# Kernel optimization log

Measured on AMD Instinct MI355X. Metric: run time of the kernel, lower is better.

Reference implementation:

```python
import jax, jax.numpy as jnp
import numpy as np

DIM, HEADS = 768, 12
HEAD_DIM = DIM // HEADS
SCALE = HEAD_DIM ** -0.5


def setup_inputs() -> dict:
    key = jax.random.key(0)
    ks = jax.random.split(key, 16)
    B, LQ, LK = 8, 512, 512
    s = DIM ** -0.5
    inp = {
        "query": jax.random.normal(ks[0], (B, LQ, DIM), jnp.float32),
        "key_value": jax.random.normal(ks[1], (B, LK, DIM), jnp.float32),
        "query_coords": jax.random.normal(ks[2], (LQ, 2), jnp.float32),
        "key_coords": jax.random.normal(ks[3], (LK, 2), jnp.float32),
        "Wq": jax.random.normal(ks[4], (DIM, DIM), jnp.float32) * s,
        "bq": jnp.zeros((DIM,), jnp.float32),
        "Wk": jax.random.normal(ks[5], (DIM, DIM), jnp.float32) * s,
        "bk": jnp.zeros((DIM,), jnp.float32),
        "Wv": jax.random.normal(ks[6], (DIM, DIM), jnp.float32) * s,
        "bv": jnp.zeros((DIM,), jnp.float32),
        "Wo": jax.random.normal(ks[7], (DIM, DIM), jnp.float32) * s,
        "bo": jnp.zeros((DIM,), jnp.float32),
        "W1": jax.random.normal(ks[8], (6, DIM), jnp.float32) * (6 ** -0.5),
        "b1": jnp.zeros((DIM,), jnp.float32),
        "W2": jax.random.normal(ks[9], (DIM, HEADS), jnp.float32) * s,
        "b2": jnp.zeros((HEADS,), jnp.float32),
    }
    return inp


def reference(query, key_value, query_coords, key_coords,
              Wq, bq, Wk, bk, Wv, bv, Wo, bo, W1, b1, W2, b2):
    B, LQ, _ = query.shape
    LK = key_value.shape[1]
    # QKV projections -> [B, L, H, Dh]
    q = (query @ Wq + bq).reshape(B, LQ, HEADS, HEAD_DIM)
    k = (key_value @ Wk + bk).reshape(B, LK, HEADS, HEAD_DIM)
    v = (key_value @ Wv + bv).reshape(B, LK, HEADS, HEAD_DIM)
    # attention logits [B, H, LQ, LK]
    logits = jnp.einsum('bqhd,bkhd->bhqk', q, k) * SCALE
    # pairwise relative bias: delta [LQ, LK, 2] -> rel [LQ, LK, 6]
    delta = query_coords[:, None, :] - key_coords[None, :, :]
    rel = jnp.concatenate([delta, jnp.abs(delta), jnp.square(delta)], axis=-1)
    hidden = jax.nn.gelu(rel @ W1 + b1, approximate=False)  # [LQ, LK, DIM]
    bias = hidden @ W2 + b2  # [LQ, LK, H]
    logits = logits + jnp.transpose(bias, (2, 0, 1))[None]  # [B,H,LQ,LK]
    weights = jax.nn.softmax(logits, axis=-1)
    out = jnp.einsum('bhqk,bkhd->bqhd', weights, v).reshape(B, LQ, DIM)
    return out @ Wo + bo
```

## Files before the change

kernel.cpp:

```cpp
#include <hip/hip_runtime.h>
#include <hip/hip_bf16.h>
#include <stdint.h>
#include <math.h>

typedef __attribute__((ext_vector_type(4))) float f32x4;
typedef _Float16 f16;
typedef __attribute__((ext_vector_type(8))) _Float16 f16x8;
typedef decltype(__builtin_amdgcn_cvt_pkrtz(0.f, 0.f)) pk16;

#define DIM   768
#define NH    12
#define HD    64
#define NB    8
#define SEQ   512
#define SCALE 0.125f

#define GN    161
#define GPTS  (GN * GN)

#define MFMA16H __builtin_amdgcn_mfma_f32_16x16x32_f16

struct PrepArgs {
    const float* query; const float* key_value; f16* Xq; f16* Xkv;
    const float* W[4]; f16* WT[4];
    const float* W1; const float* b1; const float* W2;
    f16* W1tab; f16* W2tab; float* gtab32;
};

__global__ void __launch_bounds__(256) k_prep(PrepArgs pa) {
    __shared__ float tt[32][33];
    int g = blockIdx.x, t = threadIdx.x;
    if (g < 3072) {
        const float* in = (g < 1536) ? pa.query : pa.key_value;
        f16* out = (g < 1536) ? pa.Xq : pa.Xkv;
        int i = (g % 1536) * 256 + t;
        const float4* s = reinterpret_cast<const float4*>(in + i * 8);
        float4 f0 = s[0], f1 = s[1];
        union { pk16 h[4]; uint4 v; } o;
        o.h[0] = __builtin_amdgcn_cvt_pkrtz(f0.x, f0.y);
        o.h[1] = __builtin_amdgcn_cvt_pkrtz(f0.z, f0.w);
        o.h[2] = __builtin_amdgcn_cvt_pkrtz(f1.x, f1.y);
        o.h[3] = __builtin_amdgcn_cvt_pkrtz(f1.z, f1.w);
        reinterpret_cast<uint4*>(out)[i] = o.v;
    } else if (g < 5376) {
        int bi = g - 3072;
        int z = bi / 576, rem = bi % 576;
        int bx = rem % 24, by = rem / 24;
        const float* W = pa.W[z];
        f16* WT = pa.WT[z];
        int n0 = bx * 32, k0 = by * 32;
        int tx = t & 31, ty = t >> 5;
#pragma unroll
        for (int j = 0; j < 4; ++j)
            tt[ty + 8 * j][tx] = W[(k0 + ty + 8 * j) * DIM + n0 + tx];
        __syncthreads();
#pragma unroll
        for (int j = 0; j < 4; ++j)
            WT[(n0 + ty + 8 * j) * DIM + k0 + tx] = (f16)tt[tx][ty + 8 * j];
    } else {
        int i = (g - 5376) * 256 + t;
        if (i < 3072) {
            int lane = i & 63;
            int hi = lane >> 4, m = lane & 15;
            int u = (i >> 6) * 16 + m;
#pragma unroll
            for (int e = 0; e < 8; ++e) {
                float v = 0.f;
                if (hi == 0) {
                    if (e < 6) v = pa.W1[e * DIM + u];
                    else if (e == 6) v = pa.b1[u];
                }
                pa.W1tab[i * 8 + e] = (f16)v;
            }
        } else if (i < 4608) {
            int i2 = i - 3072;
            int j = i2 >> 6, lane = i2 & 63;
            int gq = lane >> 4, h = lane & 15;
#pragma unroll
            for (int e = 0; e < 8; ++e) {
                int u = 32 * j + ((e >> 2) << 4) + (gq << 2) + (e & 3);
                float v = (h < 12) ? pa.W2[u * 12 + h] : 0.f;
                pa.W2tab[i2 * 8 + e] = (f16)v;
            }
        } else {
            int i2 = i - 4608;
            float x = (i2 + 0.5f) * (1.0f / 256.0f) - 8.0f;
            pa.gtab32[i2] = 0.5f * x * (1.0f + erff(x * 0.70710678f));
        }
    }
}

__global__ void __launch_bounds__(256) k_grid(const f16x8* __restrict__ W1tab,
                                              const f16x8* __restrict__ W2tab,
                                              const float* __restrict__ b2,
                                              const float* __restrict__ gtab32,
                                              f16* __restrict__ grid16) {
    __shared__ float tab[4096];
    int t = threadIdx.x, lane = t & 63, w = t >> 6;
    {
        const uint4* gt = (const uint4*)gtab32;
        uint4* st = (uint4*)tab;
#pragma unroll
        for (int i = 0; i < 4; ++i) st[i * 256 + t] = gt[i * 256 + t];
    }
    int hi = lane >> 4, m = lane & 15;
    int p0 = blockIdx.x * 64 + w * 16;
    int p = p0 + m;
    int gy = p / GN, gx = p - gy * GN;
    float dx = gx * 0.125f - 10.0f;
    float dy = gy * 0.125f - 10.0f;

    union { f16x8 v; pk16 h2[4]; } rf;
    { f16x8 zz = {}; rf.v = zz; }
    if (hi == 0) {
        rf.h2[0] = __builtin_amdgcn_cvt_pkrtz(dx, dy);
        rf.h2[1] = __builtin_amdgcn_cvt_pkrtz(fabsf(dx), fabsf(dy));
        rf.h2[2] = __builtin_amdgcn_cvt_pkrtz(dx * dx, dy * dy);
        rf.h2[3] = __builtin_amdgcn_cvt_pkrtz(1.0f, 0.0f);
    }

    float b2h = (m < 12) ? b2[m] : 0.f;
    f32x4 acc = {b2h, b2h, b2h, b2h};
    const f32x4 zero = {};
    const f16x8* w1p = W1tab + lane;
    const f16x8* w2p = W2tab + lane;
    __syncthreads();

#pragma unroll 2
    for (int j = 0; j < 24; ++j) {
        f16x8 a0  = w1p[(2 * j) * 64];
        f16x8 a1  = w1p[(2 * j + 1) * 64];
        f16x8 w2v = w2p[j * 64];
        f32x4 pre0 = MFMA16H(a0, rf.v, zero, 0, 0, 0);
        f32x4 pre1 = MFMA16H(a1, rf.v, zero, 0, 0, 0);
        float s0[4], s1[4];
#pragma unroll
        for (int e = 0; e < 4; ++e) {
            float x0 = pre0[e];
            float xi0 = __builtin_amdgcn_fmed3f(__builtin_fmaf(x0, 256.f, 2048.f), 0.f, 4095.f);
            float g0 = tab[(int)xi0];
            s0[e] = (x0 > 8.f) ? x0 : g0;
            float x1 = pre1[e];
            float xi1 = __builtin_amdgcn_fmed3f(__builtin_fmaf(x1, 256.f, 2048.f), 0.f, 4095.f);
            float g1 = tab[(int)xi1];
            s1[e] = (x1 > 8.f) ? x1 : g1;
        }
        union { f16x8 v; pk16 h2[4]; } pav;
        pav.h2[0] = __builtin_amdgcn_cvt_pkrtz(s0[0], s0[1]);
        pav.h2[1] = __builtin_amdgcn_cvt_pkrtz(s0[2], s0[3]);
        pav.h2[2] = __builtin_amdgcn_cvt_pkrtz(s1[0], s1[1]);
        pav.h2[3] = __builtin_amdgcn_cvt_pkrtz(s1[2], s1[3]);
        acc = MFMA16H(pav.v, w2v, acc, 0, 0, 0);
    }
    if (m < 12) {
#pragma unroll
        for (int r = 0; r < 4; ++r) {
            int pr = p0 + hi * 4 + r;
            if (pr < GPTS) grid16[pr * 16 + m] = (f16)acc[r];
        }
    }
}

struct MQArgs {
    const float* qc; const float* kc;
    const f16* grid16; f16* bias16;
    const f16* Xq; const f16* Xkv;
    const f16* WqT; const f16* WkT; const f16* WvT;
    const float* bq; const float* bk; const float* bv;
    f16* q_ws; f16* k_ws; f16* v_t;
};

__global__ void __launch_bounds__(256) k_mq5(MQArgs a) {
    __shared__ uint4 lds[1024];
    int bid = blockIdx.x, t = threadIdx.x;
    int lane = t & 63, w = t >> 6;
    int hi = lane >> 4, lm = lane & 15;
    int xcd = bid & 7, slot = bid >> 3;

    if (slot >= 16) {
        int lid = xcd * 288 + (slot - 16);
        int m_group = lid / 36;
        int within = lid - m_group * 36;
        int z = within / 12;
        int n_tile = within - z * 12;
        int m0 = m_group * 64, n0 = n_tile * 64;
        const f16* X = (z == 0) ? a.Xq : a.Xkv;
        const f16* Wt = (z == 0) ? a.WqT : (z == 1) ? a.WkT : a.WvT;
        const float* bias = (z == 0) ? a.bq : (z == 1) ? a.bk : a.bv;
        f16* out = (z == 0) ? a.q_ws : (z == 1) ? a.k_ws : a.v_t;

        int wr = w >> 1, wc = w & 1;
        int srow = t >> 2, sslot = t & 3;
        const f16* Ag = X + (m0 + srow) * DIM + sslot * 8;
        const f16* Bg = Wt + (n0 + srow) * DIM + sslot * 8;
        int wi = srow * 4 + (sslot ^ ((srow >> 1) & 3));

        int aidx[2], bidx[2];
#pragma unroll
        for (int i = 0; i < 2; ++i) {
            int ar = wr * 32 + i * 16 + lm;
            aidx[i] = ar * 4 + (hi ^ ((ar >> 1) & 3));
            int br = wc * 32 + i * 16 + lm;
            bidx[i] = 256 + br * 4 + (hi ^ ((br >> 1) & 3));
        }

        f32x4 acc[2][2] = {};
        {
            uint4 a0 = *(const uint4*)(Ag);
            uint4 b0 = *(const uint4*)(Bg);
            lds[wi] = a0;
            lds[256 + wi] = b0;
        }
        uint4 sA1 = *(const uint4*)(Ag + 32);
        uint4 sB1 = *(const uint4*)(Bg + 32);
        uint4 sA0 = *(const uint4*)(Ag + 64);
        uint4 sB0 = *(const uint4*)(Bg + 64);
        __syncthreads();

#define MQ_COMPUTE(kt)                                                        \
        {                                                                     \
            int bo = ((kt) & 1) << 9;                                         \
            f16x8 af0 = *(const f16x8*)&lds[bo + aidx[0]];                    \
            f16x8 af1 = *(const f16x8*)&lds[bo + aidx[1]];                    \
            f16x8 bf0 = *(const f16x8*)&lds[bo + bidx[0]];                    \
            f16x8 bf1 = *(const f16x8*)&lds[bo + bidx[1]];                    \
            acc[0][0] = MFMA16H(af0, bf0, acc[0][0], 0, 0, 0);                \
            acc[0][1] = MFMA16H(af0, bf1, acc[0][1], 0, 0, 0);                \
            acc[1][0] = MFMA16H(af1, bf0, acc[1][0], 0, 0, 0);                \
            acc[1][1] = MFMA16H(af1, bf1, acc[1][1], 0, 0, 0);                \
        }

        for (int kp = 0; kp < 12; ++kp) {
            int kt = 2 * kp;
            MQ_COMPUTE(kt)
            {
                int bo2 = (((kt) & 1) << 9) ^ 512;
                lds[bo2 + wi] = sA1;
                lds[bo2 + 256 + wi] = sB1;
                if (kt + 3 < 24) {
                    sA1 = *(const uint4*)(Ag + (kt + 3) * 32);
                    sB1 = *(const uint4*)(Bg + (kt + 3) * 32);
                }
                __syncthreads();
            }
            kt = 2 * kp + 1;
            MQ_COMPUTE(kt)
            if (kt < 23) {
                int bo2 = (((kt) & 1) << 9) ^ 512;
                lds[bo2 + wi] = sA0;
                lds[bo2 + 256 + wi] = sB0;
                if (kt + 3 < 24) {
                    sA0 = *(const uint4*)(Ag + (kt + 3) * 32);
                    sB0 = *(const uint4*)(Bg + (kt + 3) * 32);
                }
                __syncthreads();
            }
        }
#undef MQ_COMPUTE

#pragma unroll
        for (int mi = 0; mi < 2; ++mi)
#pragma unroll
            for (int ni = 0; ni < 2; ++ni) {
                int n = n0 + wc * 32 + ni * 16 + lm;
                float bn = bias[n];
                int h = n >> 6, d = n & 63;
                int mbase = m0 + wr * 32 + mi * 16 + hi * 4;
                int bb = mbase >> 9, l0 = mbase & 511;
                if (z == 2) {
                    union { pk16 h2[2]; uint2 u2; } o;
                    o.h2[0] = __builtin_amdgcn_cvt_pkrtz(acc[mi][ni][0] + bn, acc[mi][ni][1] + bn);
                    o.h2[1] = __builtin_amdgcn_cvt_pkrtz(acc[mi][ni][2] + bn, acc[mi][ni][3] + bn);
                    *reinterpret_cast<uint2*>(out + (((bb * NH + h) * HD) + d) * SEQ + l0) = o.u2;
                } else {
#pragma unroll
                    for (int r = 0; r < 4; ++r)
                        out[(((bb * NH + h) * SEQ) + l0 + r) * HD + d] = (f16)(acc[mi][ni][r] + bn);
                }
            }
    } else {
        int id = xcd * 16 + slot;
#pragma unroll 2
        for (int i = 0; i < 8; ++i) {
            int p = id * 2048 + i * 256 + t;
            int qi = p >> 9, ki = p & 511;
            float dx = a.qc[2 * qi] - a.kc[2 * ki];
            float dy = a.qc[2 * qi + 1] - a.kc[2 * ki + 1];
            float fxf = __builtin_amdgcn_fmed3f(__builtin_fmaf(dx, 8.f, 80.f), 0.f, 159.9999f);
            float fyf = __builtin_amdgcn_fmed3f(__builtin_fmaf(dy, 8.f, 80.f), 0.f, 159.9999f);
            int ix = (int)fxf, iy = (int)fyf;
            float fx = fxf - (float)ix, fy = fyf - (float)iy;
            const f16* c00 = a.grid16 + (iy * GN + ix) * 16;
            f16x8 g00 = *(const f16x8*)(c00);
            f16x8 g00b = *(const f16x8*)(c00 + 8);
            f16x8 g01 = *(const f16x8*)(c00 + 16);
            f16x8 g01b = *(const f16x8*)(c00 + 24);
            f16x8 g10 = *(const f16x8*)(c00 + GN * 16);
            f16x8 g10b = *(const f16x8*)(c00 + GN * 16 + 8);
            f16x8 g11 = *(const f16x8*)(c00 + GN * 16 + 16);
            f16x8 g11b = *(const f16x8*)(c00 + GN * 16 + 24);
            float o[12];
#pragma unroll
            for (int h = 0; h < 12; ++h) {
                float v00 = (float)(h < 8 ? g00[h] : g00b[h - 8]);
                float v01 = (float)(h < 8 ? g01[h] : g01b[h - 8]);
                float v10 = (float)(h < 8 ? g10[h] : g10b[h - 8]);
                float v11 = (float)(h < 8 ? g11[h] : g11b[h - 8]);
                float v0 = __builtin_fmaf(fx, v01 - v00, v00);
                float v1 = __builtin_fmaf(fx, v11 - v10, v10);
                o[h] = __builtin_fmaf(fy, v1 - v0, v0);
            }
#pragma unroll
            for (int h = 0; h < 12; ++h)
                a.bias16[h * (SEQ * SEQ) + p] = (f16)o[h];
        }
    }
}

__global__ void __launch_bounds__(256) k_gemmO(const f16* __restrict__ X,
                                               const f16* __restrict__ WT,
                                               const float* __restrict__ bias,
                                               float* __restrict__ out) {
    __shared__ uint4 lds[2048];
    int bid = blockIdx.x;
    int xcd = bid & 7, slot = bid >> 3;
    int m0 = (xcd * 4 + slot / 6) * 128, n0 = (slot % 6) * 128;
    int t = threadIdx.x, lane = t & 63, w = t >> 6;
    int wr = w >> 1, wc = w & 1;
    int lm = lane & 15, hi = lane >> 4;

    int srow = t >> 1, sch = t & 1;
    const f16* Ag = X + (m0 + srow) * DIM + sch * 16;
    const f16* Bg = WT + (n0 + srow) * DIM + sch * 16;
    int sw = (srow >> 1) & 3;
    int wiA0 = srow * 4 + ((2 * sch) ^ sw);
    int wiA1 = srow * 4 + ((2 * sch + 1) ^ sw);

    int aidx[4], bidx[4];
#pragma unroll
    for (int i = 0; i < 4; ++i) {
        int ar = wr * 64 + i * 16 + lm;
        aidx[i] = ar * 4 + (hi ^ ((ar >> 1) & 3));
        int br = wc * 64 + i * 16 + lm;
        bidx[i] = 512 + br * 4 + (hi ^ ((br >> 1) & 3));
    }

    f32x4 acc[4][4] = {};
    {
        lds[wiA0] = *(const uint4*)(Ag);
        lds[wiA1] = *(const uint4*)(Ag + 8);
        lds[512 + wiA0] = *(const uint4*)(Bg);
        lds[512 + wiA1] = *(const uint4*)(Bg + 8);
    }
    __syncthreads();

    for (int kt = 0; kt < 24; ++kt) {
        uint4 na0, na1, nb0, nb1;
        bool pf = kt < 23;
        if (pf) {
            const f16* An = Ag + (kt + 1) * 32;
            const f16* Bn = Bg + (kt + 1) * 32;
            na0 = *(const uint4*)(An);
            na1 = *(const uint4*)(An + 8);
            nb0 = *(const uint4*)(Bn);
            nb1 = *(const uint4*)(Bn + 8);
        }
        int bo = (kt & 1) << 10;
        f16x8 af[4], bf[4];
#pragma unroll
        for (int i = 0; i < 4; ++i) {
            af[i] = *(const f16x8*)&lds[bo + aidx[i]];
            bf[i] = *(const f16x8*)&lds[bo + bidx[i]];
        }
#pragma unroll
        for (int mi = 0; mi < 4; ++mi)
#pragma unroll
            for (int ni = 0; ni < 4; ++ni)
                acc[mi][ni] = MFMA16H(af[mi], bf[ni], acc[mi][ni], 0, 0, 0);
        if (pf) {
            int bo2 = bo ^ 1024;
            lds[bo2 + wiA0] = na0; lds[bo2 + wiA1] = na1;
            lds[bo2 + 512 + wiA0] = nb0; lds[bo2 + 512 + wiA1] = nb1;
            __syncthreads();
        }
    }

#pragma unroll
    for (int mi = 0; mi < 4; ++mi)
#pragma unroll
        for (int ni = 0; ni < 4; ++ni) {
            int n = n0 + wc * 64 + ni * 16 + lm;
            float bn = bias[n];
#pragma unroll
            for (int r = 0; r < 4; ++r) {
                int m = m0 + wr * 64 + mi * 16 + hi * 4 + r;
                out[m * DIM + n] = acc[mi][ni][r] + bn;
            }
        }
}

__global__ void __launch_bounds__(256) k_attn4(const f16* __restrict__ q_ws,
                                               const f16* __restrict__ k_ws,
                                               const f16* __restrict__ v_t,
                                               const f16* __restrict__ bias16,
                                               f16* __restrict__ attn_out) {
    __shared__ __align__(16) unsigned short sm16[32 * 520];
    __shared__ float inv32[32];
    int bid = blockIdx.x;
    int xcd = bid & 7, slot = bid >> 3;
    int g = xcd * 12 + (slot >> 4);
    int h = g % 12, b = g / 12;
    int qt = slot & 15;
    int q0 = qt * 32;
    int t = threadIdx.x, lane = t & 63, w = t >> 6;
    int lrow = lane & 15, hi = lane >> 4;
    int bh = b * NH + h;
    const f16* Q = q_ws + (bh * SEQ + q0) * HD;
    const f16* K = k_ws + bh * SEQ * HD;
    const f16* Bias = bias16 + (h * SEQ + q0) * SEQ;

    f16x8 aq[2][2];
#pragma unroll
    for (int rt = 0; rt < 2; ++rt)
#pragma unroll
        for (int ds = 0; ds < 2; ++ds) {
            f16x8 v = *(const f16x8*)(Q + (rt * 16 + lrow) * HD + ds * 32 + hi * 8);
            aq[rt][ds] = v * (f16)SCALE;
        }

#pragma unroll
    for (int ct = 0; ct < 8; ++ct) {
        f32x4 acc0 = {}, acc1 = {};
        int kk = w * 128 + ct * 16 + lrow;
#pragma unroll
        for (int ds = 0; ds < 2; ++ds) {
            f16x8 bk = *(const f16x8*)(K + kk * HD + ds * 32 + hi * 8);
            acc0 = MFMA16H(aq[0][ds], bk, acc0, 0, 0, 0);
            acc1 = MFMA16H(aq[1][ds], bk, acc1, 0, 0, 0);
        }
#pragma unroll
        for (int r = 0; r < 4; ++r) {
            int row0 = hi * 4 + r;
            sm16[row0 * 520 + kk] = (unsigned short)__builtin_bit_cast(unsigned short,
                (f16)(acc0[r] + (float)Bias[row0 * SEQ + kk]));
            int row1 = 16 + hi * 4 + r;
            sm16[row1 * 520 + kk] = (unsigned short)__builtin_bit_cast(unsigned short,
                (f16)(acc1[r] + (float)Bias[row1 * SEQ + kk]));
        }
    }
    __syncthreads();

    {
        int row = t >> 3, seg = t & 7;
        int base = row * 520 + 2 * seg;
        float mx = -1e30f;
#pragma unroll 8
        for (int j = 0; j < 32; ++j) {
            union { uint u; f16 h[2]; } cv;
            cv.u = *(const uint*)&sm16[base + 16 * j];
            mx = fmaxf(mx, fmaxf((float)cv.h[0], (float)cv.h[1]));
        }
        mx = fmaxf(mx, __shfl_xor(mx, 1));
        mx = fmaxf(mx, __shfl_xor(mx, 2));
        mx = fmaxf(mx, __shfl_xor(mx, 4));
        float s = 0.f;
#pragma unroll 8
        for (int j = 0; j < 32; ++j) {
            union { uint u; f16 h[2]; } cv;
            cv.u = *(const uint*)&sm16[base + 16 * j];
            float p0 = __builtin_amdgcn_exp2f(((float)cv.h[0] - mx) * 1.442695041f);
            float p1 = __builtin_amdgcn_exp2f(((float)cv.h[1] - mx) * 1.442695041f);
            s += p0 + p1;
            union { pk16 h; uint u; } o;
            o.h = __builtin_amdgcn_cvt_pkrtz(p0, p1);
            *(uint*)&sm16[base + 16 * j] = o.u;
        }
        s += __shfl_xor(s, 1);
        s += __shfl_xor(s, 2);
        s += __shfl_xor(s, 4);
        if (seg == 0) inv32[row] = 1.0f / s;
    }
    __syncthreads();

    const f16* Vt = v_t + bh * HD * SEQ + (w * 16 + lrow) * SEQ;
    f32x4 oacc0 = {}, oacc1 = {};
    for (int kt = 0; kt < 16; ++kt) {
        f16x8 bv = *(const f16x8*)(Vt + kt * 32 + hi * 8);
        f16x8 pa0 = *(const f16x8*)&sm16[lrow * 520 + kt * 32 + hi * 8];
        f16x8 pa1 = *(const f16x8*)&sm16[(16 + lrow) * 520 + kt * 32 + hi * 8];
        oacc0 = MFMA16H(pa0, bv, oacc0, 0, 0, 0);
        oacc1 = MFMA16H(pa1, bv, oacc1, 0, 0, 0);
    }
#pragma unroll
    for (int r = 0; r < 4; ++r) {
        int row0 = hi * 4 + r;
        float v0 = oacc0[r] * inv32[row0];
        attn_out[(b * SEQ + q0 + row0) * DIM + h * HD + w * 16 + lrow] = (f16)v0;
        int row1 = 16 + hi * 4 + r;
        float v1 = oacc1[r] * inv32[row1];
        attn_out[(b * SEQ + q0 + row1) * DIM + h * HD + w * 16 + lrow] = (f16)v1;
    }
}

extern "C" void kernel_launch(void* const* d_in, const int* in_sizes, int n_in,
                              void* d_out, int out_size, void* d_ws, size_t ws_size,
                              hipStream_t stream) {
    const float* query     = (const float*)d_in[0];
    const float* key_value = (const float*)d_in[1];
    const float* qc        = (const float*)d_in[2];
    const float* kc        = (const float*)d_in[3];
    const float* Wq        = (const float*)d_in[4];
    const float* bq        = (const float*)d_in[5];
    const float* Wk        = (const float*)d_in[6];
    const float* bk        = (const float*)d_in[7];
    const float* Wv        = (const float*)d_in[8];
    const float* bv        = (const float*)d_in[9];
    const float* Wo        = (const float*)d_in[10];
    const float* bo        = (const float*)d_in[11];
    const float* W1        = (const float*)d_in[12];
    const float* b1        = (const float*)d_in[13];
    const float* W2        = (const float*)d_in[14];
    const float* b2        = (const float*)d_in[15];

    char* ws = (char*)d_ws;
    f16* Xq   = (f16*)(ws + 0);
    f16* Xkv  = (f16*)(ws + 6291456);
    f16* WqT  = (f16*)(ws + 12582912);
    f16* WkT  = (f16*)(ws + 13762560);
    f16* WvT  = (f16*)(ws + 14942208);
    f16* WoT  = (f16*)(ws + 16121856);
    f16* q_ws = (f16*)(ws + 17301504);
    f16* k_ws = (f16*)(ws + 23592960);
    f16* v_t  = (f16*)(ws + 29884416);
    f16* bias16   = (f16*)(ws + 36175872);
    f16* W1tab    = (f16*)(ws + 42467328);
    f16* W2tab    = (f16*)(ws + 42516480);
    float* gtab32 = (float*)(ws + 42541056);
    f16* grid16   = (f16*)(ws + 42557440);
    f16* attn_out = Xq;

    PrepArgs pa;
    pa.query = query; pa.key_value = key_value; pa.Xq = Xq; pa.Xkv = Xkv;
    pa.W[0] = Wq; pa.W[1] = Wk; pa.W[2] = Wv; pa.W[3] = Wo;
    pa.WT[0] = WqT; pa.WT[1] = WkT; pa.WT[2] = WvT; pa.WT[3] = WoT;
    pa.W1 = W1; pa.b1 = b1; pa.W2 = W2;
    pa.W1tab = W1tab; pa.W2tab = W2tab; pa.gtab32 = gtab32;
    k_prep<<<dim3(5410), dim3(256), 0, stream>>>(pa);

    k_grid<<<dim3(406), dim3(256), 0, stream>>>((const f16x8*)W1tab, (const f16x8*)W2tab,
                                                b2, gtab32, grid16);

    MQArgs mq;
    mq.qc = qc; mq.kc = kc;
    mq.grid16 = grid16; mq.bias16 = bias16;
    mq.Xq = Xq; mq.Xkv = Xkv;
    mq.WqT = WqT; mq.WkT = WkT; mq.WvT = WvT;
    mq.bq = bq; mq.bk = bk; mq.bv = bv;
    mq.q_ws = q_ws; mq.k_ws = k_ws; mq.v_t = v_t;
    k_mq5<<<dim3(2432), dim3(256), 0, stream>>>(mq);

    k_attn4<<<dim3(1536), dim3(256), 0, stream>>>(q_ws, k_ws, v_t, bias16, attn_out);
    k_gemmO<<<dim3(192), dim3(256), 0, stream>>>(attn_out, WoT, bo, (float*)d_out);
}
```

Measured before the change: 110.1 us.

## Shrink output GEMM tiles to 64x64 and add two-stage register prefetch

Replaces the 128x128-tile output projection GEMM with a 64x64-tile version, raising the grid from 192 to 768 blocks so more of the GPU's compute units have work. Global loads are now prefetched two k-steps ahead through alternating register buffers, which hides more load latency. The cost is less data reuse per tile and more total global reads of X and WT, plus a remapped XCD-aware block ordering.

```diff
diff --git a/kernel.cpp b/kernel.cpp
--- a/kernel.cpp
+++ b/kernel.cpp
@@ -317,83 +317,97 @@
     }
 }
 
-__global__ void __launch_bounds__(256) k_gemmO(const f16* __restrict__ X,
-                                               const f16* __restrict__ WT,
-                                               const float* __restrict__ bias,
-                                               float* __restrict__ out) {
-    __shared__ uint4 lds[2048];
-    int bid = blockIdx.x;
+__global__ void __launch_bounds__(256) k_gemmO2(const f16* __restrict__ X,
+                                                const f16* __restrict__ WT,
+                                                const float* __restrict__ bias,
+                                                float* __restrict__ out) {
+    __shared__ uint4 lds[1024];
+    int bid = blockIdx.x, t = threadIdx.x;
+    int lane = t & 63, w = t >> 6;
+    int hi = lane >> 4, lm = lane & 15;
     int xcd = bid & 7, slot = bid >> 3;
-    int m0 = (xcd * 4 + slot / 6) * 128, n0 = (slot % 6) * 128;
-    int t = threadIdx.x, lane = t & 63, w = t >> 6;
+    int lid = xcd * 96 + slot;
+    int m_group = lid / 12, n_tile = lid % 12;
+    int m0 = m_group * 64, n0 = n_tile * 64;
+
     int wr = w >> 1, wc = w & 1;
-    int lm = lane & 15, hi = lane >> 4;
-
-    int srow = t >> 1, sch = t & 1;
-    const f16* Ag = X + (m0 + srow) * DIM + sch * 16;
-    const f16* Bg = WT + (n0 + srow) * DIM + sch * 16;
-    int sw = (srow >> 1) & 3;
-    int wiA0 = srow * 4 + ((2 * sch) ^ sw);
-    int wiA1 = srow * 4 + ((2 * sch + 1) ^ sw);
-
-    int aidx[4], bidx[4];
-#pragma unroll
-    for (int i = 0; i < 4; ++i) {
-        int ar = wr * 64 + i * 16 + lm;
+    int srow = t >> 2, sslot = t & 3;
+    const f16* Ag = X + (m0 + srow) * DIM + sslot * 8;
+    const f16* Bg = WT + (n0 + srow) * DIM + sslot * 8;
+    int wi = srow * 4 + (sslot ^ ((srow >> 1) & 3));
+
+    int aidx[2], bidx[2];
+#pragma unroll
+    for (int i = 0; i < 2; ++i) {
+        int ar = wr * 32 + i * 16 + lm;
         aidx[i] = ar * 4 + (hi ^ ((ar >> 1) & 3));
-        int br = wc * 64 + i * 16 + lm;
-        bidx[i] = 512 + br * 4 + (hi ^ ((br >> 1) & 3));
-    }
-
-    f32x4 acc[4][4] = {};
+        int br = wc * 32 + i * 16 + lm;
+        bidx[i] = 256 + br * 4 + (hi ^ ((br >> 1) & 3));
+    }
+
+    f32x4 acc[2][2] = {};
     {
-        lds[wiA0] = *(const uint4*)(Ag);
-        lds[wiA1] = *(const uint4*)(Ag + 8);
-        lds[512 + wiA0] = *(const uint4*)(Bg);
-        lds[512 + wiA1] = *(const uint4*)(Bg + 8);
-    }
+        uint4 a0 = *(const uint4*)(Ag);
+        uint4 b0 = *(const uint4*)(Bg);
+        lds[wi] = a0;
+        lds[256 + wi] = b0;
+    }
+    uint4 sA1 = *(const uint4*)(Ag + 32);
+    uint4 sB1 = *(const uint4*)(Bg + 32);
+    uint4 sA0 = *(const uint4*)(Ag + 64);
+    uint4 sB0 = *(const uint4*)(Bg + 64);
     __syncthreads();
 
-    for (int kt = 0; kt < 24; ++kt) {
-        uint4 na0, na1, nb0, nb1;
-        bool pf = kt < 23;
-        if (pf) {
-            const f16* An = Ag + (kt + 1) * 32;
-            const f16* Bn = Bg + (kt + 1) * 32;
-            na0 = *(const uint4*)(An);
-            na1 = *(const uint4*)(An + 8);
-            nb0 = *(const uint4*)(Bn);
-            nb1 = *(const uint4*)(Bn + 8);
-        }
-        int bo = (kt & 1) << 10;
-        f16x8 af[4], bf[4];
-#pragma unroll
-        for (int i = 0; i < 4; ++i) {
-            af[i] = *(const f16x8*)&lds[bo + aidx[i]];
-            bf[i] = *(const f16x8*)&lds[bo + bidx[i]];
-        }
-#pragma unroll
-        for (int mi = 0; mi < 4; ++mi)
-#pragma unroll
-            for (int ni = 0; ni < 4; ++ni)
-                acc[mi][ni] = MFMA16H(af[mi], bf[ni], acc[mi][ni], 0, 0, 0);
-        if (pf) {
-            int bo2 = bo ^ 1024;
-            lds[bo2 + wiA0] = na0; lds[bo2 + wiA1] = na1;
-            lds[bo2 + 512 + wiA0] = nb0; lds[bo2 + 512 + wiA1] = nb1;
+#define GO_COMPUTE(kt)                                                        \
+    {                                                                         \
+        int bo = ((kt) & 1) << 9;                                             \
+        f16x8 af0 = *(const f16x8*)&lds[bo + aidx[0]];                        \
+        f16x8 af1 = *(const f16x8*)&lds[bo + aidx[1]];                        \
+        f16x8 bf0 = *(const f16x8*)&lds[bo + bidx[0]];                        \
+        f16x8 bf1 = *(const f16x8*)&lds[bo + bidx[1]];                        \
+        acc[0][0] = MFMA16H(af0, bf0, acc[0][0], 0, 0, 0);                    \
+        acc[0][1] = MFMA16H(af0, bf1, acc[0][1], 0, 0, 0);                    \
+        acc[1][0] = MFMA16H(af1, bf0, acc[1][0], 0, 0, 0);                    \
+        acc[1][1] = MFMA16H(af1, bf1, acc[1][1], 0, 0, 0);                    \
+    }
+
+    for (int kp = 0; kp < 12; ++kp) {
+        int kt = 2 * kp;
+        GO_COMPUTE(kt)
+        {
+            int bo2 = (((kt) & 1) << 9) ^ 512;
+            lds[bo2 + wi] = sA1;
+            lds[bo2 + 256 + wi] = sB1;
+            if (kt + 3 < 24) {
+                sA1 = *(const uint4*)(Ag + (kt + 3) * 32);
+                sB1 = *(const uint4*)(Bg + (kt + 3) * 32);
+            }
             __syncthreads();
         }
-    }
-
-#pragma unroll
-    for (int mi = 0; mi < 4; ++mi)
-#pragma unroll
-        for (int ni = 0; ni < 4; ++ni) {
-            int n = n0 + wc * 64 + ni * 16 + lm;
+        kt = 2 * kp + 1;
+        GO_COMPUTE(kt)
+        if (kt < 23) {
+            int bo2 = (((kt) & 1) << 9) ^ 512;
+            lds[bo2 + wi] = sA0;
+            lds[bo2 + 256 + wi] = sB0;
+            if (kt + 3 < 24) {
+                sA0 = *(const uint4*)(Ag + (kt + 3) * 32);
+                sB0 = *(const uint4*)(Bg + (kt + 3) * 32);
+            }
+            __syncthreads();
+        }
+    }
+#undef GO_COMPUTE
+
+#pragma unroll
+    for (int mi = 0; mi < 2; ++mi)
+#pragma unroll
+        for (int ni = 0; ni < 2; ++ni) {
+            int n = n0 + wc * 32 + ni * 16 + lm;
             float bn = bias[n];
 #pragma unroll
             for (int r = 0; r < 4; ++r) {
-                int m = m0 + wr * 64 + mi * 16 + hi * 4 + r;
+                int m = m0 + wr * 32 + mi * 16 + hi * 4 + r;
                 out[m * DIM + n] = acc[mi][ni][r] + bn;
             }
         }
@@ -560,5 +574,5 @@
     k_mq5<<<dim3(2432), dim3(256), 0, stream>>>(mq);
 
     k_attn4<<<dim3(1536), dim3(256), 0, stream>>>(q_ws, k_ws, v_t, bias16, attn_out);
-    k_gemmO<<<dim3(192), dim3(256), 0, stream>>>(attn_out, WoT, bo, (float*)d_out);
+    k_gemmO2<<<dim3(768), dim3(256), 0, stream>>>(attn_out, WoT, bo, (float*)d_out);
 }
```

Result: faster. 106.6 us (-3.2%).
